# Performance work log

Hardware: AMD Instinct MI355X
Metric: run time of the kernel (lower is better)

## Reference

```python
import jax, jax.numpy as jnp
import numpy as np
from jax import lax

B, C, H, W = 8, 256, 64, 64
O, K, E = 256, 3, 3  # out_channels, kernel_size, num_experts

def setup_inputs() -> dict:
    key = jax.random.key(0)
    k1, k2, k3, k4, k5 = jax.random.split(key, 5)
    q = jax.random.normal(k1, (B, C, H, W), dtype=jnp.float32)
    y = jax.random.normal(k2, (B, C, H, W), dtype=jnp.float32)
    experts = jax.random.normal(k3, (E, O, 2 * C, K, K), dtype=jnp.float32)
    # torch nn.Linear(2C, E): store transposed [2C, E] for ctx @ gate_w
    bound = 1.0 / np.sqrt(2 * C)
    gate_w = jax.random.uniform(k4, (2 * C, E), minval=-bound, maxval=bound, dtype=jnp.float32)
    gate_b = jax.random.uniform(k5, (E,), minval=-bound, maxval=bound, dtype=jnp.float32)
    return {"q": q, "y": y, "experts": experts, "gate_w": gate_w, "gate_b": gate_b}

def reference(q, y, experts, gate_w, gate_b):
    # gate: softmax over experts from global-avg-pooled context of y (duplicated)
    y_ctx = jnp.mean(y, axis=(2, 3))                       # [B, C]
    context = jnp.concatenate([y_ctx, y_ctx], axis=1)       # [B, 2C]
    gates = jax.nn.softmax(context @ gate_w + gate_b, axis=1)  # [B, E]
    # per-sample fused kernel: sum_e gates[b,e] * experts[e]  -> [B, O, 2C, K, K]
    w = jnp.einsum('be,eoikl->boikl', gates, experts)
    xy = jnp.concatenate([q, q], axis=1)                     # [B, 2C, H, W]
    # batched dynamic conv via grouped conv: batch -> groups (no Python loop)
    b, c2, h, wd = xy.shape
    x1 = xy.reshape(1, b * c2, h, wd)
    w1 = w.reshape(b * O, c2, K, K)
    out = lax.conv_general_dilated(
        x1, w1, window_strides=(1, 1), padding='SAME',
        dimension_numbers=('NCHW', 'OIHW', 'NCHW'),
        feature_group_count=b)
    return out.reshape(b, O, h, wd)
```

## Files before the change

kernel.cpp:

```cpp
#include <hip/hip_runtime.h>
#include <hip/hip_bf16.h>
#include <math.h>


typedef __bf16 bf16x8 __attribute__((ext_vector_type(8)));
typedef __bf16 bf16x4 __attribute__((ext_vector_type(4)));
typedef float f32x4 __attribute__((ext_vector_type(4)));

#define AS1 __attribute__((address_space(1)))
#define AS3 __attribute__((address_space(3)))

__global__ __launch_bounds__(64) void yctx_kernel(const float* __restrict__ y,
                                                  float* __restrict__ yctx) {
  int bc = blockIdx.x;
  const float4* p = (const float4*)(y + (size_t)bc * 4096);
  int lane = threadIdx.x;
  float s = 0.f;
  for (int i = lane; i < 1024; i += 64) {
    float4 v = p[i];
    s += v.x + v.y + v.z + v.w;
  }
#pragma unroll
  for (int off = 32; off > 0; off >>= 1) s += __shfl_down(s, off, 64);
  if (lane == 0) yctx[bc] = s * (1.f / 4096.f);
}

__global__ __launch_bounds__(64) void logits_kernel(const float* __restrict__ yctx,
                                                    const float* __restrict__ gw,
                                                    const float* __restrict__ gb,
                                                    float* __restrict__ logits) {
  int be = blockIdx.x;
  int b = be / 3, e = be - b * 3;
  int lane = threadIdx.x;
  float s = 0.f;
  for (int c = lane; c < 256; c += 64)
    s += yctx[b * 256 + c] * (gw[c * 3 + e] + gw[(c + 256) * 3 + e]);
#pragma unroll
  for (int off = 32; off > 0; off >>= 1) s += __shfl_down(s, off, 64);
  if (lane == 0) logits[be] = s + gb[e];
}

__global__ __launch_bounds__(256) void wbuild_kernel(const float* __restrict__ experts,
                                                     const float* __restrict__ logits,
                                                     __bf16* __restrict__ wf) {
  int o = blockIdx.x;
  int tid = threadIdx.x;
  __shared__ float sf[3][2304];
  __shared__ float g[8][3];

#pragma unroll
  for (int e = 0; e < 3; e++) {
    const float4* src = (const float4*)(experts + ((size_t)e * 256 + o) * 4608);
    float4* dstp = (float4*)sf[e];
    for (int i = tid; i < 576; i += 256) {
      float4 a = src[i], bq = src[i + 576];
      float4 r;
      r.x = a.x + bq.x; r.y = a.y + bq.y; r.z = a.z + bq.z; r.w = a.w + bq.w;
      dstp[i] = r;
    }
  }
  if (tid < 8) {
    float l0 = logits[tid * 3 + 0], l1 = logits[tid * 3 + 1], l2 = logits[tid * 3 + 2];
    float m = fmaxf(l0, fmaxf(l1, l2));
    float e0 = __expf(l0 - m), e1 = __expf(l1 - m), e2 = __expf(l2 - m);
    float inv = 1.f / (e0 + e1 + e2);
    g[tid][0] = e0 * inv; g[tid][1] = e1 * inv; g[tid][2] = e2 * inv;
  }
  __syncthreads();

  int cl = tid & 31, ch = tid >> 5;
#pragma unroll 1
  for (int b = 0; b < 8; b++) {
    float g0 = g[b][0], g1 = g[b][1], g2 = g[b][2];
#pragma unroll
    for (int tap = 0; tap < 9; tap++) {
      float v = g0 * sf[0][tid * 9 + tap] + g1 * sf[1][tid * 9 + tap] +
                g2 * sf[2][tid * 9 + tap];
      wf[((((size_t)b * 9 + tap) * 8 + ch) * 256 + o) * 32 + cl] = (__bf16)v;
    }
  }
}

__global__ __launch_bounds__(256) void qt_kernel(const float* __restrict__ q,
                                                 __bf16* __restrict__ qT) {
  int bid = blockIdx.x;
  int hp = bid % 66;
  int t2 = bid / 66;
  int ch = t2 & 7;
  int b = t2 >> 3;
  __bf16* dst = qT + (((size_t)(b * 8 + ch) * 66 + hp) * 66) * 32;
  int tid = threadIdx.x;
  float4 z4 = {0.f, 0.f, 0.f, 0.f};
  if (hp == 0 || hp == 65) {
    float4* d4 = (float4*)dst;
    for (int i = tid; i < 264; i += 256) d4[i] = z4;
    return;
  }
  __shared__ float tile2[64][33];
  int h = hp - 1;
  {
    int w = tid & 63, ci = tid >> 6;
#pragma unroll
    for (int j = 0; j < 8; j++) {
      int c = ci * 8 + j;
      tile2[w][c] = q[(((size_t)b * 256 + ch * 32 + c) * 64 + h) * 64 + w];
    }
  }
  if (tid < 4) ((float4*)dst)[tid] = z4;
  else if (tid < 8) ((float4*)(dst + 65 * 32))[tid - 4] = z4;
  __syncthreads();

  int a = tid & 7, wsl = tid >> 3;
  int cl4 = a * 4;
#pragma unroll
  for (int k = 0; k < 2; k++) {
    int w = wsl * 2 + k, wp = w + 1;
    int clp4 = (((cl4 >> 3) ^ ((wp >> 1) & 3)) << 3) | (cl4 & 7);
    float v0 = tile2[w][cl4 + 0], v1 = tile2[w][cl4 + 1];
    float v2 = tile2[w][cl4 + 2], v3 = tile2[w][cl4 + 3];
    bf16x4 r = {(__bf16)v0, (__bf16)v1, (__bf16)v2, (__bf16)v3};
    *(bf16x4*)(dst + wp * 32 + clp4) = r;
  }
}

__global__ __launch_bounds__(256) void conv_kernel(const __bf16* __restrict__ qT,
                                                   const __bf16* __restrict__ wf,
                                                   float* __restrict__ out) {
  __shared__ __align__(16) __bf16 Qlds[2][4 * 66 * 32];
  const int tid = threadIdx.x;
  const int lane = tid & 63;
  const int wv = tid >> 6;
  const int wm = wv >> 1, wn = wv & 1;
  const int l15 = lane & 15, qd = lane >> 4;

  const int bid = blockIdx.x;
  const int b = bid & 7;
  const int rem = bid >> 3;
  const int o0 = (rem >> 5) * 128;
  const int h0 = (rem & 31) * 2;

  f32x4 acc[4][4];
  {
    f32x4 z = {0.f, 0.f, 0.f, 0.f};
#pragma unroll
    for (int i = 0; i < 4; i++)
#pragma unroll
      for (int j = 0; j < 4; j++) acc[i][j] = z;
  }

  const char* qT_b = (const char*)qT + (size_t)b * 8 * 66 * 66 * 32 * 2;
  const char* abase = (const char*)wf + ((size_t)b * 9 * 8 * 256 +
                                         (size_t)(o0 + wm * 64 + l15)) * 64 +
                      (size_t)qd * 16;
  bf16x8 acur[4], anxt[4];

  {
    const char* qsrc = qT_b + ((size_t)h0) * 66 * 32 * 2;
    for (int i = tid; i < 1056; i += 256) {
      int ub = i - lane;
      __builtin_amdgcn_global_load_lds((const AS1 void*)(qsrc + ((size_t)i << 4)),
                                       (AS3 void*)((char*)Qlds[0] + ((size_t)ub << 4)),
                                       16, 0, 0);
    }
#pragma unroll
    for (int mi = 0; mi < 4; mi++)
      acur[mi] = *(const bf16x8*)(abase + mi * 1024);
    __syncthreads();
  }

#pragma unroll 1
  for (int ch = 0; ch < 8; ch++) {
    if (ch < 7) {
      const char* qsrc = qT_b + ((size_t)(ch + 1) * 66 + h0) * 66 * 32 * 2;
      char* qdst = (char*)Qlds[(ch + 1) & 1];
      for (int i = tid; i < 1056; i += 256) {
        int ub = i - lane;
        __builtin_amdgcn_global_load_lds((const AS1 void*)(qsrc + ((size_t)i << 4)),
                                         (AS3 void*)(qdst + ((size_t)ub << 4)),
                                         16, 0, 0);
      }
    }
    const char* Qb = (const char*)Qlds[ch & 1];
#pragma unroll
    for (int tap = 0; tap < 9; tap++) {
      {
        int tapn = (tap == 8) ? 0 : tap + 1;
        int chn = (tap == 8) ? ch + 1 : ch;
        size_t aoff = ((size_t)(tapn * 8 + chn)) << 14;
#pragma unroll
        for (int mi = 0; mi < 4; mi++)
          anxt[mi] = *(const bf16x8*)(abase + aoff + mi * 1024);
      }
      const int dh = tap / 3, dw = tap - dh * 3;
      const int r = wn + dh;
#pragma unroll
      for (int ni = 0; ni < 4; ni++) {
        int wp = ni * 16 + l15 + dw;
        int g = (qd ^ ((wp >> 1) & 3)) << 3;
        bf16x8 bfv = *(const bf16x8*)(Qb + ((r * 66 + wp) * 32 + g) * 2);
#pragma unroll
        for (int mi = 0; mi < 4; mi++)
          acc[mi][ni] = __builtin_amdgcn_mfma_f32_16x16x32_bf16(
              acur[mi], bfv, acc[mi][ni], 0, 0, 0);
      }
#pragma unroll
      for (int mi = 0; mi < 4; mi++) acur[mi] = anxt[mi];
    }
    __syncthreads();
  }

  const int hh = h0 + wn;
#pragma unroll
  for (int mi = 0; mi < 4; mi++) {
    int o = o0 + wm * 64 + mi * 16 + qd * 4;
#pragma unroll
    for (int ni = 0; ni < 4; ni++) {
      int w = ni * 16 + l15;
#pragma unroll
      for (int rr = 0; rr < 4; rr++)
        out[(((size_t)b * 256 + (o + rr)) * 64 + hh) * 64 + w] = acc[mi][ni][rr];
    }
  }
}

extern "C" void kernel_launch(void* const* d_in, const int* in_sizes, int n_in,
                              void* d_out, int out_size, void* d_ws, size_t ws_size,
                              hipStream_t stream) {
  (void)in_sizes; (void)n_in; (void)out_size; (void)ws_size;
  const float* q = (const float*)d_in[0];
  const float* y = (const float*)d_in[1];
  const float* experts = (const float*)d_in[2];
  const float* gate_w = (const float*)d_in[3];
  const float* gate_b = (const float*)d_in[4];
  float* out = (float*)d_out;

  char* ws = (char*)d_ws;
  float* yctx = (float*)ws;
  float* logits = (float*)(ws + 8192);
  __bf16* wf = (__bf16*)(ws + 16384);
  __bf16* qT = (__bf16*)(ws + 16384 + 9437184);

  yctx_kernel<<<2048, 64, 0, stream>>>(y, yctx);
  logits_kernel<<<24, 64, 0, stream>>>(yctx, gate_w, gate_b, logits);
  qt_kernel<<<8 * 8 * 66, 256, 0, stream>>>(q, qT);
  wbuild_kernel<<<256, 256, 0, stream>>>(experts, logits, wf);
  conv_kernel<<<512, 256, 0, stream>>>(qT, wf, out);
}
```

Baseline: 178.3 us.

## Enlarge conv tile to 4 rows, fuse logits into wbuild, vectorize weight stores

The conv kernel now computes 4 output rows per block instead of 2, doubling the accumulator tiles per wave so each A-fragment load feeds twice as many MFMAs. The grid is halved to 256 blocks and the LDS buffer is enlarged for the 6 halo rows. The logits kernel is removed and its work folded into wbuild, saving one launch. wbuild writes bf16x4 vectors instead of scalars. Risks: higher register pressure, and 256 blocks may leave some CUs idle on a 256-CU part.

```diff
diff --git a/kernel.cpp b/kernel.cpp
--- a/kernel.cpp
+++ b/kernel.cpp
@@ -25,28 +25,16 @@
   if (lane == 0) yctx[bc] = s * (1.f / 4096.f);
 }
 
-__global__ __launch_bounds__(64) void logits_kernel(const float* __restrict__ yctx,
-                                                    const float* __restrict__ gw,
-                                                    const float* __restrict__ gb,
-                                                    float* __restrict__ logits) {
-  int be = blockIdx.x;
-  int b = be / 3, e = be - b * 3;
-  int lane = threadIdx.x;
-  float s = 0.f;
-  for (int c = lane; c < 256; c += 64)
-    s += yctx[b * 256 + c] * (gw[c * 3 + e] + gw[(c + 256) * 3 + e]);
-#pragma unroll
-  for (int off = 32; off > 0; off >>= 1) s += __shfl_down(s, off, 64);
-  if (lane == 0) logits[be] = s + gb[e];
-}
-
 __global__ __launch_bounds__(256) void wbuild_kernel(const float* __restrict__ experts,
-                                                     const float* __restrict__ logits,
+                                                     const float* __restrict__ yctx,
+                                                     const float* __restrict__ gw,
+                                                     const float* __restrict__ gb,
                                                      __bf16* __restrict__ wf) {
   int o = blockIdx.x;
   int tid = threadIdx.x;
   __shared__ float sf[3][2304];
   __shared__ float g[8][3];
+  __shared__ float lg[24];
 
 #pragma unroll
   for (int e = 0; e < 3; e++) {
@@ -59,8 +47,16 @@
       dstp[i] = r;
     }
   }
+  if (tid < 24) {
+    int b = tid / 3, e = tid - b * 3;
+    float s = gb[e];
+    for (int c = 0; c < 256; c++)
+      s += yctx[b * 256 + c] * (gw[c * 3 + e] + gw[(c + 256) * 3 + e]);
+    lg[tid] = s;
+  }
+  __syncthreads();
   if (tid < 8) {
-    float l0 = logits[tid * 3 + 0], l1 = logits[tid * 3 + 1], l2 = logits[tid * 3 + 2];
+    float l0 = lg[tid * 3 + 0], l1 = lg[tid * 3 + 1], l2 = lg[tid * 3 + 2];
     float m = fmaxf(l0, fmaxf(l1, l2));
     float e0 = __expf(l0 - m), e1 = __expf(l1 - m), e2 = __expf(l2 - m);
     float inv = 1.f / (e0 + e1 + e2);
@@ -68,16 +64,20 @@
   }
   __syncthreads();
 
-  int cl = tid & 31, ch = tid >> 5;
+  int grp = tid >> 6, ch = (tid >> 3) & 7, clq = tid & 7;
 #pragma unroll 1
-  for (int b = 0; b < 8; b++) {
+  for (int bt = grp; bt < 72; bt += 4) {
+    int b = bt / 9, tap = bt - b * 9;
     float g0 = g[b][0], g1 = g[b][1], g2 = g[b][2];
-#pragma unroll
-    for (int tap = 0; tap < 9; tap++) {
-      float v = g0 * sf[0][tid * 9 + tap] + g1 * sf[1][tid * 9 + tap] +
-                g2 * sf[2][tid * 9 + tap];
-      wf[((((size_t)b * 9 + tap) * 8 + ch) * 256 + o) * 32 + cl] = (__bf16)v;
-    }
+    bf16x4 r;
+#pragma unroll
+    for (int j = 0; j < 4; j++) {
+      int c = ch * 32 + clq * 4 + j;
+      float v = g0 * sf[0][c * 9 + tap] + g1 * sf[1][c * 9 + tap] +
+                g2 * sf[2][c * 9 + tap];
+      r[j] = (__bf16)v;
+    }
+    *(bf16x4*)(wf + ((((size_t)b * 9 + tap) * 8 + ch) * 256 + o) * 32 + clq * 4) = r;
   }
 }
 
@@ -123,10 +123,10 @@
   }
 }
 
-__global__ __launch_bounds__(256) void conv_kernel(const __bf16* __restrict__ qT,
-                                                   const __bf16* __restrict__ wf,
-                                                   float* __restrict__ out) {
-  __shared__ __align__(16) __bf16 Qlds[2][4 * 66 * 32];
+__global__ __launch_bounds__(256, 1) void conv_kernel(const __bf16* __restrict__ qT,
+                                                      const __bf16* __restrict__ wf,
+                                                      float* __restrict__ out) {
+  __shared__ __align__(16) char Qlds[2][28672];
   const int tid = threadIdx.x;
   const int lane = tid & 63;
   const int wv = tid >> 6;
@@ -136,16 +136,16 @@
   const int bid = blockIdx.x;
   const int b = bid & 7;
   const int rem = bid >> 3;
-  const int o0 = (rem >> 5) * 128;
-  const int h0 = (rem & 31) * 2;
-
-  f32x4 acc[4][4];
+  const int o0 = (rem >> 4) * 128;
+  const int h0 = (rem & 15) * 4;
+
+  f32x4 acc[4][8];
   {
     f32x4 z = {0.f, 0.f, 0.f, 0.f};
 #pragma unroll
     for (int i = 0; i < 4; i++)
 #pragma unroll
-      for (int j = 0; j < 4; j++) acc[i][j] = z;
+      for (int j = 0; j < 8; j++) acc[i][j] = z;
   }
 
   const char* qT_b = (const char*)qT + (size_t)b * 8 * 66 * 66 * 32 * 2;
@@ -155,11 +155,12 @@
   bf16x8 acur[4], anxt[4];
 
   {
-    const char* qsrc = qT_b + ((size_t)h0) * 66 * 32 * 2;
-    for (int i = tid; i < 1056; i += 256) {
+    const char* qsrc = qT_b + ((size_t)h0) * 4224;
+    for (int i = tid; i < 1792; i += 256) {
+      int gi = (i < 1584) ? i : 0;
       int ub = i - lane;
-      __builtin_amdgcn_global_load_lds((const AS1 void*)(qsrc + ((size_t)i << 4)),
-                                       (AS3 void*)((char*)Qlds[0] + ((size_t)ub << 4)),
+      __builtin_amdgcn_global_load_lds((const AS1 void*)(qsrc + ((size_t)gi << 4)),
+                                       (AS3 void*)(Qlds[0] + ((size_t)ub << 4)),
                                        16, 0, 0);
     }
 #pragma unroll
@@ -171,16 +172,17 @@
 #pragma unroll 1
   for (int ch = 0; ch < 8; ch++) {
     if (ch < 7) {
-      const char* qsrc = qT_b + ((size_t)(ch + 1) * 66 + h0) * 66 * 32 * 2;
-      char* qdst = (char*)Qlds[(ch + 1) & 1];
-      for (int i = tid; i < 1056; i += 256) {
+      const char* qsrc = qT_b + ((size_t)((ch + 1) * 66 + h0)) * 4224;
+      char* qdst = Qlds[(ch + 1) & 1];
+      for (int i = tid; i < 1792; i += 256) {
+        int gi = (i < 1584) ? i : 0;
         int ub = i - lane;
-        __builtin_amdgcn_global_load_lds((const AS1 void*)(qsrc + ((size_t)i << 4)),
+        __builtin_amdgcn_global_load_lds((const AS1 void*)(qsrc + ((size_t)gi << 4)),
                                          (AS3 void*)(qdst + ((size_t)ub << 4)),
                                          16, 0, 0);
       }
     }
-    const char* Qb = (const char*)Qlds[ch & 1];
+    const char* Qb = Qlds[ch & 1];
 #pragma unroll
     for (int tap = 0; tap < 9; tap++) {
       {
@@ -192,10 +194,10 @@
           anxt[mi] = *(const bf16x8*)(abase + aoff + mi * 1024);
       }
       const int dh = tap / 3, dw = tap - dh * 3;
-      const int r = wn + dh;
-#pragma unroll
-      for (int ni = 0; ni < 4; ni++) {
-        int wp = ni * 16 + l15 + dw;
+#pragma unroll
+      for (int ni = 0; ni < 8; ni++) {
+        int r = wn * 2 + (ni >> 2) + dh;
+        int wp = (ni & 3) * 16 + l15 + dw;
         int g = (qd ^ ((wp >> 1) & 3)) << 3;
         bf16x8 bfv = *(const bf16x8*)(Qb + ((r * 66 + wp) * 32 + g) * 2);
 #pragma unroll
@@ -209,16 +211,16 @@
     __syncthreads();
   }
 
-  const int hh = h0 + wn;
 #pragma unroll
   for (int mi = 0; mi < 4; mi++) {
     int o = o0 + wm * 64 + mi * 16 + qd * 4;
 #pragma unroll
-    for (int ni = 0; ni < 4; ni++) {
-      int w = ni * 16 + l15;
+    for (int ni = 0; ni < 8; ni++) {
+      int h = h0 + wn * 2 + (ni >> 2);
+      int w = (ni & 3) * 16 + l15;
 #pragma unroll
       for (int rr = 0; rr < 4; rr++)
-        out[(((size_t)b * 256 + (o + rr)) * 64 + hh) * 64 + w] = acc[mi][ni][rr];
+        out[(((size_t)b * 256 + (o + rr)) * 64 + h) * 64 + w] = acc[mi][ni][rr];
     }
   }
 }
@@ -236,13 +238,11 @@
 
   char* ws = (char*)d_ws;
   float* yctx = (float*)ws;
-  float* logits = (float*)(ws + 8192);
   __bf16* wf = (__bf16*)(ws + 16384);
   __bf16* qT = (__bf16*)(ws + 16384 + 9437184);
 
   yctx_kernel<<<2048, 64, 0, stream>>>(y, yctx);
-  logits_kernel<<<24, 64, 0, stream>>>(yctx, gate_w, gate_b, logits);
   qt_kernel<<<8 * 8 * 66, 256, 0, stream>>>(q, qT);
-  wbuild_kernel<<<256, 256, 0, stream>>>(experts, logits, wf);
-  conv_kernel<<<512, 256, 0, stream>>>(qT, wf, out);
-}
+  wbuild_kernel<<<256, 256, 0, stream>>>(experts, yctx, gate_w, gate_b, wf);
+  conv_kernel<<<256, 256, 0, stream>>>(qT, wf, out);
+}
```

Result: slower. 190.5 us (+6.9%).
